# Kernel tuning notes

Measured on AMD Instinct MI355X. Metric: run time of the kernel, lower is better.

The kernel has to match this reference:

```python
import jax, jax.numpy as jnp
import numpy as np

SEM_ENC_DIM = 1024
SENT_HIDDEN_DIM = 1024
ATT_DIM = 512

def setup_inputs() -> dict:
    key = jax.random.key(0)
    ks = jax.random.split(key, 8)
    B, L = 64, 2048
    s = lambda d: 1.0 / np.sqrt(d)
    return {
        "sem_enc_output": jax.random.normal(ks[0], (B, L, SEM_ENC_DIM), dtype=jnp.float32),
        "dec_hidden_state": jax.random.normal(ks[1], (B, SENT_HIDDEN_DIM), dtype=jnp.float32),
        "W_enc": jax.random.uniform(ks[2], (SEM_ENC_DIM, ATT_DIM), jnp.float32, -s(SEM_ENC_DIM), s(SEM_ENC_DIM)),
        "b_enc": jax.random.uniform(ks[3], (ATT_DIM,), jnp.float32, -s(SEM_ENC_DIM), s(SEM_ENC_DIM)),
        "W_dec": jax.random.uniform(ks[4], (SENT_HIDDEN_DIM, ATT_DIM), jnp.float32, -s(SENT_HIDDEN_DIM), s(SENT_HIDDEN_DIM)),
        "b_dec": jax.random.uniform(ks[5], (ATT_DIM,), jnp.float32, -s(SENT_HIDDEN_DIM), s(SENT_HIDDEN_DIM)),
        "W_full": jax.random.uniform(ks[6], (ATT_DIM, 1), jnp.float32, -s(ATT_DIM), s(ATT_DIM)),
        "b_full": jax.random.uniform(ks[7], (1,), jnp.float32, -s(ATT_DIM), s(ATT_DIM)),
    }

def reference(sem_enc_output, dec_hidden_state, W_enc, b_enc, W_dec, b_dec, W_full, b_full):
    # enc projection: [B, L, att_dim]
    enc_proj = jnp.einsum('ble,ea->bla', sem_enc_output, W_enc) + b_enc
    # dec projection: [B, att_dim]
    dec_proj = dec_hidden_state @ W_dec + b_dec
    # broadcast add + tanh: [B, L, att_dim]
    joined = jnp.tanh(enc_proj + dec_proj[:, None, :])
    # scoring: [B, L]
    scores = (jnp.einsum('bla,a->bl', joined, W_full[:, 0]) + b_full[0])
    att_scores = jax.nn.softmax(scores, axis=1)
    # weighted sum over L of the PROJECTED encoder output (matches torch code)
    att_output = jnp.einsum('bl,bla->ba', att_scores, enc_proj)
    return (att_output, att_scores)
```

## Files before the change

kernel.cpp:

```cpp
#include <hip/hip_runtime.h>
#include <hip/hip_bf16.h>
#include <cstdint>
#include <cstddef>

#define BB   64
#define LL   2048
#define ED   1024
#define AD   512
#define BM   128
#define BK   32
#define NCH  (LL / BM)
#define KST  (ED / BK)

typedef short  short8  __attribute__((ext_vector_type(8)));
typedef float  f32x4   __attribute__((ext_vector_type(4)));

__device__ __forceinline__ unsigned short f2bf(float x) {
  unsigned u = __float_as_uint(x);
  u += 0x7FFFu + ((u >> 16) & 1u);
  return (unsigned short)(u >> 16);
}

#define GLOAD_LDS16(gp, lp)                                                        \
  __builtin_amdgcn_global_load_lds(                                                \
      (const __attribute__((address_space(1))) unsigned int*)(gp),                 \
      (__attribute__((address_space(3))) unsigned int*)(lp), 16, 0, 0)

__global__ __launch_bounds__(512) void prep_kernel(
    const float* __restrict__ W_enc, const float* __restrict__ dec,
    const float* __restrict__ W_dec, const float* __restrict__ b_dec,
    unsigned short* __restrict__ Wb, float* __restrict__ dp) {
  const int blk = blockIdx.x, t = threadIdx.x;
  if (blk < BB) {
    const float* drow = dec + blk * ED;
    float a0 = 0.f, a1 = 0.f, a2 = 0.f, a3 = 0.f;
    for (int k = 0; k < ED; k += 4) {
      a0 = fmaf(drow[k],     W_dec[(k)     * AD + t], a0);
      a1 = fmaf(drow[k + 1], W_dec[(k + 1) * AD + t], a1);
      a2 = fmaf(drow[k + 2], W_dec[(k + 2) * AD + t], a2);
      a3 = fmaf(drow[k + 3], W_dec[(k + 3) * AD + t], a3);
    }
    dp[blk * AD + t] = (a0 + a1) + (a2 + a3) + b_dec[t];
  } else {
    const int base = (blk - BB) * 4096;
#pragma unroll
    for (int ii = 0; ii < 8; ii++) {
      const int o  = base + ii * 512 + t;
      const int ks = o >> 14;
      const int i  = (o >> 12) & 3;
      const int w  = (o >> 9) & 7;
      const int l  = (o >> 3) & 63;
      const int j  = o & 7;
      const int k  = ks * 32 + ((l >> 4) << 3) + j;
      const int c  = ((i * 8 + w) << 4) + (l & 15);
      Wb[o] = f2bf(W_enc[k * AD + c]);
    }
  }
}

__global__ __launch_bounds__(512, 2) void fused_kernel(
    const float* __restrict__ sem, const unsigned short* __restrict__ Wb,
    const float* __restrict__ dp, const float* __restrict__ b_enc,
    const float* __restrict__ Wf,
    float* __restrict__ raw_scores,
    float* __restrict__ ws_ms, float* __restrict__ ws_o) {

  __shared__ unsigned short Alds[2][4096];
  __shared__ unsigned short Blds[2][16384];

  const int t    = threadIdx.x;
  const int lane = t & 63;
  const int wave = t >> 6;
  const int wm   = wave >> 2;
  const int wn   = wave & 3;
  const int b    = blockIdx.y;
  const int chunk= blockIdx.x;
  const int l0   = chunk * BM;

  const int srow = t >> 2;
  const int skg  = t & 3;
  const float* aptr = sem + ((size_t)(b * LL + l0 + srow)) * ED + skg * 8;
  const unsigned short* bsrc = Wb + t * 8;
  const int awr = (srow >> 4) * 512 + skg * 128 + (srow & 15) * 8;

  const int arow = lane & 15;
  const int akg  = lane >> 4;
  const int afr  = wm * 4 * 512 + lane * 8;
  const int bfr  = wn * 8 * 512 + lane * 8;

  f32x4 acc[4][8];
#pragma unroll
  for (int i = 0; i < 4; i++)
#pragma unroll
    for (int j = 0; j < 8; j++) acc[i][j] = (f32x4)0.f;

#pragma unroll
  for (int i = 0; i < 4; i++)
    GLOAD_LDS16(bsrc + i * 4096, &Blds[0][i * 4096 + t * 8]);
  f32x4 pA0 = *(const f32x4*)(aptr);
  f32x4 pA1 = *(const f32x4*)(aptr + 4);
  f32x4 qA0 = *(const f32x4*)(aptr + BK);
  f32x4 qA1 = *(const f32x4*)(aptr + BK + 4);
  {
    short8 aw;
    aw[0]=(short)f2bf(pA0[0]); aw[1]=(short)f2bf(pA0[1]); aw[2]=(short)f2bf(pA0[2]); aw[3]=(short)f2bf(pA0[3]);
    aw[4]=(short)f2bf(pA1[0]); aw[5]=(short)f2bf(pA1[1]); aw[6]=(short)f2bf(pA1[2]); aw[7]=(short)f2bf(pA1[3]);
    *(short8*)&Alds[0][awr] = aw;
  }
  asm volatile("s_waitcnt vmcnt(2) lgkmcnt(0)" ::: "memory");
  __builtin_amdgcn_sched_barrier(0);
  __builtin_amdgcn_s_barrier();

#define ITER(ks, CA0, CA1, LA0, LA1)                                              \
  {                                                                               \
    const int cb = (ks) & 1, nb = ((ks) + 1) & 1;                                 \
    if ((ks) + 1 < KST) {                      \
      const unsigned short* bs = bsrc + ((ks) + 1) * 16384;                       \
      _Pragma("unroll")                                                           \
      for (int i = 0; i < 4; i++)                                                 \
        GLOAD_LDS16(bs + i * 4096, &Blds[nb][i * 4096 + t * 8]);                  \
    }                                                                             \
    __builtin_amdgcn_sched_barrier(0);      \
    if ((ks) + 1 < KST) {                                                         \
      short8 aw;                                                                  \
      aw[0]=(short)f2bf(CA0[0]); aw[1]=(short)f2bf(CA0[1]);                       \
      aw[2]=(short)f2bf(CA0[2]); aw[3]=(short)f2bf(CA0[3]);                       \
      aw[4]=(short)f2bf(CA1[0]); aw[5]=(short)f2bf(CA1[1]);                       \
      aw[6]=(short)f2bf(CA1[2]); aw[7]=(short)f2bf(CA1[3]);                       \
      *(short8*)&Alds[nb][awr] = aw;                                              \
    }                                                                             \
    if ((ks) + 2 < KST) {                                                         \
      const float* ap = aptr + ((ks) + 2) * BK;                                   \
      LA0 = *(const f32x4*)(ap);                                                  \
      LA1 = *(const f32x4*)(ap + 4);                                              \
    }                                                                             \
    short8 av[4], bv[8];                                                          \
    _Pragma("unroll")                                                             \
    for (int mf = 0; mf < 4; mf++)                                                \
      av[mf] = *(const short8*)&Alds[cb][afr + mf * 512];                         \
    _Pragma("unroll")                                                             \
    for (int nf = 0; nf < 8; nf++)                                                \
      bv[nf] = *(const short8*)&Blds[cb][bfr + nf * 512];                         \
    __builtin_amdgcn_s_setprio(1);                                                \
    _Pragma("unroll")                                                             \
    for (int mf = 0; mf < 4; mf++)                                                \
      _Pragma("unroll")                                                           \
      for (int nf = 0; nf < 8; nf++)                                              \
        acc[mf][nf] = __builtin_amdgcn_mfma_f32_16x16x32_bf16(av[mf], bv[nf], acc[mf][nf], 0, 0, 0); \
    __builtin_amdgcn_s_setprio(0);                                                \
    if ((ks) + 2 < KST) {                 \
      asm volatile("s_waitcnt vmcnt(2) lgkmcnt(0)" ::: "memory");                 \
    } else {                                                                      \
      asm volatile("s_waitcnt vmcnt(0) lgkmcnt(0)" ::: "memory");                 \
    }                                                                             \
    __builtin_amdgcn_sched_barrier(0);                                            \
    __builtin_amdgcn_s_barrier();                                                 \
  }

  for (int kk = 0; kk < KST; kk += 2) {
    ITER(kk,     qA0, qA1, pA0, pA1);
    ITER(kk + 1, pA0, pA1, qA0, qA1);
  }
#undef ITER

  float* eb = (float*)&Blds[0][0];
  float (*sc_part)[4]   = (float (*)[4])eb;
  float* scores_lds     = eb + 512;
  float* weight         = eb + 640;
  float (*o_lds)[AD]    = (float (*)[AD])(eb + 768);
  float* bcv            = eb + 1792;

  float dpv[8], wfv[8], bev[8];
#pragma unroll
  for (int nf = 0; nf < 8; nf++) {
    const int c = wn * 128 + nf * 16 + arow;
    dpv[nf] = dp[b * AD + c];
    wfv[nf] = Wf[c];
    bev[nf] = b_enc[c];
  }
#pragma unroll
  for (int mf = 0; mf < 4; mf++) {
#pragma unroll
    for (int r = 0; r < 4; r++) {
      float p = 0.f;
#pragma unroll
      for (int nf = 0; nf < 8; nf++) {
        float e = acc[mf][nf][r] + bev[nf];
        acc[mf][nf][r] = e;
        float x = e + dpv[nf];
        float ex = __expf(2.f * x);
        float th = 1.f - 2.f / (ex + 1.f);
        p = fmaf(th, wfv[nf], p);
      }
      p += __shfl_xor(p, 1); p += __shfl_xor(p, 2);
      p += __shfl_xor(p, 4); p += __shfl_xor(p, 8);
      if (arow == 0) sc_part[wm * 64 + mf * 16 + akg * 4 + r][wn] = p;
    }
  }
  __syncthreads();

  if (t < BM) {
    float s = sc_part[t][0] + sc_part[t][1] + sc_part[t][2] + sc_part[t][3];
    scores_lds[t] = s;
    raw_scores[(size_t)b * LL + l0 + t] = s;
  }
  __syncthreads();
  if (t < 64) {
    float m = fmaxf(scores_lds[t], scores_lds[t + 64]);
#pragma unroll
    for (int off = 1; off < 64; off <<= 1) m = fmaxf(m, __shfl_xor(m, off));
    if (t == 0) bcv[0] = m;
  }
  __syncthreads();
  const float m_c = bcv[0];
  if (t < BM) weight[t] = __expf(scores_lds[t] - m_c);
  __syncthreads();
  if (t < 64) {
    float s = weight[t] + weight[t + 64];
#pragma unroll
    for (int off = 1; off < 64; off <<= 1) s += __shfl_xor(s, off);
    if (t == 0) bcv[1] = s;
  }

  float wv[4][4];
#pragma unroll
  for (int mf = 0; mf < 4; mf++)
#pragma unroll
    for (int r = 0; r < 4; r++) wv[mf][r] = weight[wm * 64 + mf * 16 + akg * 4 + r];
#pragma unroll
  for (int nf = 0; nf < 8; nf++) {
    float cp = 0.f;
#pragma unroll
    for (int mf = 0; mf < 4; mf++)
#pragma unroll
      for (int r = 0; r < 4; r++) cp = fmaf(wv[mf][r], acc[mf][nf][r], cp);
    cp += __shfl_xor(cp, 16);
    cp += __shfl_xor(cp, 32);
    if (lane < 16) o_lds[wm][wn * 128 + nf * 16 + lane] = cp;
  }
  __syncthreads();
  if (t < AD)
    ws_o[((size_t)b * NCH + chunk) * AD + t] = o_lds[0][t] + o_lds[1][t];
  if (t == 0) {
    ws_ms[(b * NCH + chunk) * 2]     = m_c;
    ws_ms[(b * NCH + chunk) * 2 + 1] = bcv[1];
  }
}

__global__ __launch_bounds__(256) void finalize_kernel(
    const float* __restrict__ ws_ms, const float* __restrict__ ws_o,
    float* __restrict__ out0, float* __restrict__ outS) {
  const int b = blockIdx.x, t = threadIdx.x;
  float ms[NCH], ss[NCH];
  float M = -1e30f;
#pragma unroll
  for (int i = 0; i < NCH; i++) {
    ms[i] = ws_ms[(b * NCH + i) * 2];
    ss[i] = ws_ms[(b * NCH + i) * 2 + 1];
    M = fmaxf(M, ms[i]);
  }
  float S = 0.f, w[NCH];
#pragma unroll
  for (int i = 0; i < NCH; i++) { w[i] = __expf(ms[i] - M); S = fmaf(ss[i], w[i], S); }
  const float invS = 1.f / S;
  for (int c = t; c < AD; c += 256) {
    float a = 0.f;
#pragma unroll
    for (int i = 0; i < NCH; i++) a = fmaf(ws_o[((size_t)b * NCH + i) * AD + c], w[i], a);
    out0[b * AD + c] = a * invS;
  }
  for (int l = t; l < LL; l += 256) {
    float r = outS[(size_t)b * LL + l];
    outS[(size_t)b * LL + l] = __expf(r - M) * invS;
  }
}

extern "C" void kernel_launch(void* const* d_in, const int* in_sizes, int n_in,
                              void* d_out, int out_size, void* d_ws, size_t ws_size,
                              hipStream_t stream) {
  const float* sem    = (const float*)d_in[0];
  const float* dec    = (const float*)d_in[1];
  const float* W_enc  = (const float*)d_in[2];
  const float* b_enc  = (const float*)d_in[3];
  const float* W_dec  = (const float*)d_in[4];
  const float* b_dec  = (const float*)d_in[5];
  const float* W_full = (const float*)d_in[6];

  float* out0 = (float*)d_out;
  float* outS = out0 + BB * AD;

  char* ws = (char*)d_ws;
  unsigned short* Wb = (unsigned short*)ws;
  float* dpw   = (float*)(ws + (1 << 20));
  float* ws_ms = (float*)(ws + (1 << 20) + (128 << 10));
  float* ws_o  = (float*)(ws + (1 << 20) + (128 << 10) + (8 << 10));

  prep_kernel<<<BB + 128, 512, 0, stream>>>(W_enc, dec, W_dec, b_dec, Wb, dpw);
  dim3 g1(NCH, BB);
  fused_kernel<<<g1, 512, 0, stream>>>(sem, Wb, dpw, b_enc, W_full, outS, ws_ms, ws_o);
  finalize_kernel<<<BB, 256, 0, stream>>>(ws_ms, ws_o, out0, outS);
}
```

Baseline: 292.0 us.

## Halve row tile to 64 with 4-wave blocks and simplify softmax epilogue

Shrinks the per-block L tile from 128 to 64 rows and the block from 8 to 4 waves, each wave now covering all 64 rows and a 128-column slice. The packed W_enc layout and the B-tile loads are reworked to match. The per-chunk softmax now runs in a single wave with shuffles, and partial outputs go straight to the workspace, dropping several block barriers and the cross-wave LDS reduction. This doubles the number of blocks and the chunk count for the finalize step, and doubles the total W_enc tile traffic from L2 relative to the A data.

```diff
diff --git a/kernel.cpp b/kernel.cpp
--- a/kernel.cpp
+++ b/kernel.cpp
@@ -7,7 +7,7 @@
 #define LL   2048
 #define ED   1024
 #define AD   512
-#define BM   128
+#define BM   64
 #define BK   32
 #define NCH  (LL / BM)
 #define KST  (ED / BK)
@@ -45,34 +45,32 @@
     const int base = (blk - BB) * 4096;
 #pragma unroll
     for (int ii = 0; ii < 8; ii++) {
-      const int o  = base + ii * 512 + t;
-      const int ks = o >> 14;
-      const int i  = (o >> 12) & 3;
-      const int w  = (o >> 9) & 7;
-      const int l  = (o >> 3) & 63;
-      const int j  = o & 7;
-      const int k  = ks * 32 + ((l >> 4) << 3) + j;
-      const int c  = ((i * 8 + w) << 4) + (l & 15);
+      const int o    = base + ii * 512 + t;
+      const int ks   = o >> 14;
+      const int cblk = (o >> 9) & 31;
+      const int kg   = (o >> 7) & 3;
+      const int r    = (o >> 3) & 15;
+      const int j    = o & 7;
+      const int k    = ks * 32 + kg * 8 + j;
+      const int c    = cblk * 16 + r;
       Wb[o] = f2bf(W_enc[k * AD + c]);
     }
   }
 }
 
-__global__ __launch_bounds__(512, 2) void fused_kernel(
+__global__ __launch_bounds__(256, 2) void fused_kernel(
     const float* __restrict__ sem, const unsigned short* __restrict__ Wb,
     const float* __restrict__ dp, const float* __restrict__ b_enc,
     const float* __restrict__ Wf,
     float* __restrict__ raw_scores,
     float* __restrict__ ws_ms, float* __restrict__ ws_o) {
 
-  __shared__ unsigned short Alds[2][4096];
+  __shared__ unsigned short Alds[2][2048];
   __shared__ unsigned short Blds[2][16384];
 
   const int t    = threadIdx.x;
   const int lane = t & 63;
-  const int wave = t >> 6;
-  const int wm   = wave >> 2;
-  const int wn   = wave & 3;
+  const int wn   = t >> 6;
   const int b    = blockIdx.y;
   const int chunk= blockIdx.x;
   const int l0   = chunk * BM;
@@ -85,7 +83,7 @@
 
   const int arow = lane & 15;
   const int akg  = lane >> 4;
-  const int afr  = wm * 4 * 512 + lane * 8;
+  const int afr  = lane * 8;
   const int bfr  = wn * 8 * 512 + lane * 8;
 
   f32x4 acc[4][8];
@@ -95,8 +93,8 @@
     for (int j = 0; j < 8; j++) acc[i][j] = (f32x4)0.f;
 
 #pragma unroll
-  for (int i = 0; i < 4; i++)
-    GLOAD_LDS16(bsrc + i * 4096, &Blds[0][i * 4096 + t * 8]);
+  for (int i = 0; i < 8; i++)
+    GLOAD_LDS16(bsrc + i * 2048, &Blds[0][i * 2048 + t * 8]);
   f32x4 pA0 = *(const f32x4*)(aptr);
   f32x4 pA1 = *(const f32x4*)(aptr + 4);
   f32x4 qA0 = *(const f32x4*)(aptr + BK);
@@ -117,10 +115,10 @@
     if ((ks) + 1 < KST) {                      \
       const unsigned short* bs = bsrc + ((ks) + 1) * 16384;                       \
       _Pragma("unroll")                                                           \
-      for (int i = 0; i < 4; i++)                                                 \
-        GLOAD_LDS16(bs + i * 4096, &Blds[nb][i * 4096 + t * 8]);                  \
-    }                                                                             \
-    __builtin_amdgcn_sched_barrier(0);      \
+      for (int i = 0; i < 8; i++)                                                 \
+        GLOAD_LDS16(bs + i * 2048, &Blds[nb][i * 2048 + t * 8]);                  \
+    }                                                                             \
+    __builtin_amdgcn_sched_barrier(0);  \
     if ((ks) + 1 < KST) {                                                         \
       short8 aw;                                                                  \
       aw[0]=(short)f2bf(CA0[0]); aw[1]=(short)f2bf(CA0[1]);                       \
@@ -164,11 +162,9 @@
 #undef ITER
 
   float* eb = (float*)&Blds[0][0];
-  float (*sc_part)[4]   = (float (*)[4])eb;
-  float* scores_lds     = eb + 512;
-  float* weight         = eb + 640;
-  float (*o_lds)[AD]    = (float (*)[AD])(eb + 768);
-  float* bcv            = eb + 1792;
+  float (*sc_part)[4] = (float (*)[4])eb;
+  float* weight       = eb + 256;
+  float* scores_lds   = eb + 320;
 
   float dpv[8], wfv[8], bev[8];
 #pragma unroll
@@ -194,39 +190,34 @@
       }
       p += __shfl_xor(p, 1); p += __shfl_xor(p, 2);
       p += __shfl_xor(p, 4); p += __shfl_xor(p, 8);
-      if (arow == 0) sc_part[wm * 64 + mf * 16 + akg * 4 + r][wn] = p;
+      if (arow == 0) sc_part[mf * 16 + akg * 4 + r][wn] = p;
     }
   }
   __syncthreads();
 
   if (t < BM) {
     float s = sc_part[t][0] + sc_part[t][1] + sc_part[t][2] + sc_part[t][3];
-    scores_lds[t] = s;
     raw_scores[(size_t)b * LL + l0 + t] = s;
+    float m = s;
+#pragma unroll
+    for (int off = 1; off < 64; off <<= 1) m = fmaxf(m, __shfl_xor(m, off));
+    float w = __expf(s - m);
+    weight[t] = w;
+    float ss = w;
+#pragma unroll
+    for (int off = 1; off < 64; off <<= 1) ss += __shfl_xor(ss, off);
+    if (t == 0) {
+      ws_ms[(b * NCH + chunk) * 2]     = m;
+      ws_ms[(b * NCH + chunk) * 2 + 1] = ss;
+    }
   }
   __syncthreads();
-  if (t < 64) {
-    float m = fmaxf(scores_lds[t], scores_lds[t + 64]);
-#pragma unroll
-    for (int off = 1; off < 64; off <<= 1) m = fmaxf(m, __shfl_xor(m, off));
-    if (t == 0) bcv[0] = m;
-  }
-  __syncthreads();
-  const float m_c = bcv[0];
-  if (t < BM) weight[t] = __expf(scores_lds[t] - m_c);
-  __syncthreads();
-  if (t < 64) {
-    float s = weight[t] + weight[t + 64];
-#pragma unroll
-    for (int off = 1; off < 64; off <<= 1) s += __shfl_xor(s, off);
-    if (t == 0) bcv[1] = s;
-  }
 
   float wv[4][4];
 #pragma unroll
   for (int mf = 0; mf < 4; mf++)
 #pragma unroll
-    for (int r = 0; r < 4; r++) wv[mf][r] = weight[wm * 64 + mf * 16 + akg * 4 + r];
+    for (int r = 0; r < 4; r++) wv[mf][r] = weight[mf * 16 + akg * 4 + r];
 #pragma unroll
   for (int nf = 0; nf < 8; nf++) {
     float cp = 0.f;
@@ -236,14 +227,8 @@
       for (int r = 0; r < 4; r++) cp = fmaf(wv[mf][r], acc[mf][nf][r], cp);
     cp += __shfl_xor(cp, 16);
     cp += __shfl_xor(cp, 32);
-    if (lane < 16) o_lds[wm][wn * 128 + nf * 16 + lane] = cp;
-  }
-  __syncthreads();
-  if (t < AD)
-    ws_o[((size_t)b * NCH + chunk) * AD + t] = o_lds[0][t] + o_lds[1][t];
-  if (t == 0) {
-    ws_ms[(b * NCH + chunk) * 2]     = m_c;
-    ws_ms[(b * NCH + chunk) * 2 + 1] = bcv[1];
+    if (lane < 16)
+      ws_o[((size_t)b * NCH + chunk) * AD + wn * 128 + nf * 16 + lane] = cp;
   }
 }
 
@@ -293,10 +278,10 @@
   unsigned short* Wb = (unsigned short*)ws;
   float* dpw   = (float*)(ws + (1 << 20));
   float* ws_ms = (float*)(ws + (1 << 20) + (128 << 10));
-  float* ws_o  = (float*)(ws + (1 << 20) + (128 << 10) + (8 << 10));
+  float* ws_o  = (float*)(ws + (1 << 20) + (144 << 10));
 
   prep_kernel<<<BB + 128, 512, 0, stream>>>(W_enc, dec, W_dec, b_dec, Wb, dpw);
   dim3 g1(NCH, BB);
-  fused_kernel<<<g1, 512, 0, stream>>>(sem, Wb, dpw, b_enc, W_full, outS, ws_ms, ws_o);
+  fused_kernel<<<g1, 256, 0, stream>>>(sem, Wb, dpw, b_enc, W_full, outS, ws_ms, ws_o);
   finalize_kernel<<<BB, 256, 0, stream>>>(ws_ms, ws_o, out0, outS);
 }
```

New measurement: 283.6 us. 2.9% less time.

## Deepen GEMM pipeline to four LDS stages for B and triple-buffered A registers

Applied to the files above, without the earlier changes.

Grows the B-tile LDS ring from two to four buffers and prefetches B three k-steps ahead. A-tile fp32 register prefetch goes from two to three sets. Explicit vmcnt waits are dropped, leaving only lgkmcnt waits before each barrier, so the code relies on compiler-inserted waits for global-to-LDS completion. The W_enc packing index math is rewritten but gives the same layout. The larger LDS footprint (about 144 KB per block) probably allows only one 512-thread block per CU instead of two, trading occupancy for deeper latency hiding.

```diff
diff --git a/kernel.cpp b/kernel.cpp
--- a/kernel.cpp
+++ b/kernel.cpp
@@ -45,14 +45,14 @@
     const int base = (blk - BB) * 4096;
 #pragma unroll
     for (int ii = 0; ii < 8; ii++) {
-      const int o  = base + ii * 512 + t;
-      const int ks = o >> 14;
-      const int i  = (o >> 12) & 3;
-      const int w  = (o >> 9) & 7;
-      const int l  = (o >> 3) & 63;
-      const int j  = o & 7;
-      const int k  = ks * 32 + ((l >> 4) << 3) + j;
-      const int c  = ((i * 8 + w) << 4) + (l & 15);
+      const int o    = base + ii * 512 + t;
+      const int ks   = o >> 14;
+      const int cblk = (o >> 9) & 31;
+      const int kg   = (o >> 7) & 3;
+      const int r    = (o >> 3) & 15;
+      const int j    = o & 7;
+      const int k    = ks * 32 + kg * 8 + j;
+      const int c    = cblk * 16 + r;
       Wb[o] = f2bf(W_enc[k * AD + c]);
     }
   }
@@ -66,7 +66,7 @@
     float* __restrict__ ws_ms, float* __restrict__ ws_o) {
 
   __shared__ unsigned short Alds[2][4096];
-  __shared__ unsigned short Blds[2][16384];
+  __shared__ unsigned short Blds[4][16384];
 
   const int t    = threadIdx.x;
   const int lane = t & 63;
@@ -85,8 +85,8 @@
 
   const int arow = lane & 15;
   const int akg  = lane >> 4;
-  const int afr  = wm * 4 * 512 + lane * 8;
-  const int bfr  = wn * 8 * 512 + lane * 8;
+  const int afr  = wm * 2048 + lane * 8;
+  const int bfr  = wn * 4096 + lane * 8;
 
   f32x4 acc[4][8];
 #pragma unroll
@@ -95,52 +95,59 @@
     for (int j = 0; j < 8; j++) acc[i][j] = (f32x4)0.f;
 
 #pragma unroll
-  for (int i = 0; i < 4; i++)
-    GLOAD_LDS16(bsrc + i * 4096, &Blds[0][i * 4096 + t * 8]);
-  f32x4 pA0 = *(const f32x4*)(aptr);
-  f32x4 pA1 = *(const f32x4*)(aptr + 4);
-  f32x4 qA0 = *(const f32x4*)(aptr + BK);
-  f32x4 qA1 = *(const f32x4*)(aptr + BK + 4);
+  for (int s = 0; s < 3; s++) {
+    const unsigned short* bs = bsrc + s * 16384;
+#pragma unroll
+    for (int i = 0; i < 4; i++)
+      GLOAD_LDS16(bs + i * 4096, &Blds[s][i * 4096 + t * 8]);
+  }
+  __builtin_amdgcn_sched_barrier(0);
+  f32x4 R0a = *(const f32x4*)(aptr);
+  f32x4 R0b = *(const f32x4*)(aptr + 4);
+  f32x4 R1a = *(const f32x4*)(aptr + BK);
+  f32x4 R1b = *(const f32x4*)(aptr + BK + 4);
+  f32x4 R2a = *(const f32x4*)(aptr + 2 * BK);
+  f32x4 R2b = *(const f32x4*)(aptr + 2 * BK + 4);
+  f32x4 R3a, R3b;
   {
     short8 aw;
-    aw[0]=(short)f2bf(pA0[0]); aw[1]=(short)f2bf(pA0[1]); aw[2]=(short)f2bf(pA0[2]); aw[3]=(short)f2bf(pA0[3]);
-    aw[4]=(short)f2bf(pA1[0]); aw[5]=(short)f2bf(pA1[1]); aw[6]=(short)f2bf(pA1[2]); aw[7]=(short)f2bf(pA1[3]);
+    aw[0]=(short)f2bf(R0a[0]); aw[1]=(short)f2bf(R0a[1]); aw[2]=(short)f2bf(R0a[2]); aw[3]=(short)f2bf(R0a[3]);
+    aw[4]=(short)f2bf(R0b[0]); aw[5]=(short)f2bf(R0b[1]); aw[6]=(short)f2bf(R0b[2]); aw[7]=(short)f2bf(R0b[3]);
     *(short8*)&Alds[0][awr] = aw;
   }
-  asm volatile("s_waitcnt vmcnt(2) lgkmcnt(0)" ::: "memory");
+  asm volatile("s_waitcnt lgkmcnt(0)" ::: "memory");
   __builtin_amdgcn_sched_barrier(0);
   __builtin_amdgcn_s_barrier();
 
-#define ITER(ks, CA0, CA1, LA0, LA1)                                              \
+#define ITER(ks, BRD, BWR, ARD, AWR, CA0, CA1, LA0, LA1)                          \
   {                                                                               \
-    const int cb = (ks) & 1, nb = ((ks) + 1) & 1;                                 \
-    if ((ks) + 1 < KST) {                      \
-      const unsigned short* bs = bsrc + ((ks) + 1) * 16384;                       \
+    if ((ks) + 3 < KST) {                                                         \
+      const unsigned short* bs = bsrc + ((ks) + 3) * 16384;                       \
       _Pragma("unroll")                                                           \
       for (int i = 0; i < 4; i++)                                                 \
-        GLOAD_LDS16(bs + i * 4096, &Blds[nb][i * 4096 + t * 8]);                  \
+        GLOAD_LDS16(bs + i * 4096, &Blds[BWR][i * 4096 + t * 8]);                 \
     }                                                                             \
-    __builtin_amdgcn_sched_barrier(0);      \
+    __builtin_amdgcn_sched_barrier(0);         \
     if ((ks) + 1 < KST) {                                                         \
       short8 aw;                                                                  \
       aw[0]=(short)f2bf(CA0[0]); aw[1]=(short)f2bf(CA0[1]);                       \
       aw[2]=(short)f2bf(CA0[2]); aw[3]=(short)f2bf(CA0[3]);                       \
       aw[4]=(short)f2bf(CA1[0]); aw[5]=(short)f2bf(CA1[1]);                       \
       aw[6]=(short)f2bf(CA1[2]); aw[7]=(short)f2bf(CA1[3]);                       \
-      *(short8*)&Alds[nb][awr] = aw;                                              \
+      *(short8*)&Alds[AWR][awr] = aw;                                             \
     }                                                                             \
-    if ((ks) + 2 < KST) {                                                         \
-      const float* ap = aptr + ((ks) + 2) * BK;                                   \
+    if ((ks) + 3 < KST) {                                                         \
+      const float* ap = aptr + ((ks) + 3) * BK;                                   \
       LA0 = *(const f32x4*)(ap);                                                  \
       LA1 = *(const f32x4*)(ap + 4);                                              \
     }                                                                             \
     short8 av[4], bv[8];                                                          \
     _Pragma("unroll")                                                             \
     for (int mf = 0; mf < 4; mf++)                                                \
-      av[mf] = *(const short8*)&Alds[cb][afr + mf * 512];                         \
+      av[mf] = *(const short8*)&Alds[ARD][afr + mf * 512];                        \
     _Pragma("unroll")                                                             \
     for (int nf = 0; nf < 8; nf++)                                                \
-      bv[nf] = *(const short8*)&Blds[cb][bfr + nf * 512];                         \
+      bv[nf] = *(const short8*)&Blds[BRD][bfr + nf * 512];                        \
     __builtin_amdgcn_s_setprio(1);                                                \
     _Pragma("unroll")                                                             \
     for (int mf = 0; mf < 4; mf++)                                                \
@@ -148,18 +155,16 @@
       for (int nf = 0; nf < 8; nf++)                                              \
         acc[mf][nf] = __builtin_amdgcn_mfma_f32_16x16x32_bf16(av[mf], bv[nf], acc[mf][nf], 0, 0, 0); \
     __builtin_amdgcn_s_setprio(0);                                                \
-    if ((ks) + 2 < KST) {                 \
-      asm volatile("s_waitcnt vmcnt(2) lgkmcnt(0)" ::: "memory");                 \
-    } else {                                                                      \
-      asm volatile("s_waitcnt vmcnt(0) lgkmcnt(0)" ::: "memory");                 \
-    }                                                                             \
+    asm volatile("s_waitcnt lgkmcnt(0)" ::: "memory");   \
     __builtin_amdgcn_sched_barrier(0);                                            \
     __builtin_amdgcn_s_barrier();                                                 \
   }
 
-  for (int kk = 0; kk < KST; kk += 2) {
-    ITER(kk,     qA0, qA1, pA0, pA1);
-    ITER(kk + 1, pA0, pA1, qA0, qA1);
+  for (int kk = 0; kk < KST; kk += 4) {
+    ITER(kk,     0, 3, 0, 1, R1a, R1b, R3a, R3b);
+    ITER(kk + 1, 1, 0, 1, 0, R2a, R2b, R0a, R0b);
+    ITER(kk + 2, 2, 1, 0, 1, R3a, R3b, R1a, R1b);
+    ITER(kk + 3, 3, 2, 1, 0, R0a, R0b, R2a, R2b);
   }
 #undef ITER
 
@@ -293,7 +298,7 @@
   unsigned short* Wb = (unsigned short*)ws;
   float* dpw   = (float*)(ws + (1 << 20));
   float* ws_ms = (float*)(ws + (1 << 20) + (128 << 10));
-  float* ws_o  = (float*)(ws + (1 << 20) + (128 << 10) + (8 << 10));
+  float* ws_o  = (float*)(ws + (1 << 20) + (144 << 10));
 
   prep_kernel<<<BB + 128, 512, 0, stream>>>(W_enc, dec, W_dec, b_dec, Wb, dpw);
   dim3 g1(NCH, BB);
```

Result: slower. 393.3 us (+34.7%).
